# Kernel tuning notes

Hardware: AMD Instinct MI355X
Metric: run time of the kernel (lower is better)

Reference implementation:

```python
import jax, jax.numpy as jnp
import numpy as np

B, S, T_MEL, D, H = 16, 512, 2048, 256, 128  # batch, src_len, mel_len, encoder_hidden, lstm hidden/dir


def setup_inputs() -> dict:
    key = jax.random.key(0)
    ks = jax.random.split(key, 10)
    sc = 0.1
    x = jax.random.normal(ks[0], (B, S, D), jnp.float32)
    src_mask = jnp.zeros((B, S), bool)
    d = jax.random.uniform(ks[1], (B, S), jnp.float32, minval=0.5, maxval=8.0)
    duration = d / jnp.sum(d, -1, keepdims=True) * T_MEL  # each row sums exactly to mel_len
    Wih0 = sc * jax.random.normal(ks[2], (2, 4 * H, D), jnp.float32)
    Whh0 = sc * jax.random.normal(ks[3], (2, 4 * H, H), jnp.float32)
    b0 = jnp.zeros((2, 4 * H), jnp.float32)
    Wih1 = sc * jax.random.normal(ks[4], (2, 4 * H, 2 * H), jnp.float32)
    Whh1 = sc * jax.random.normal(ks[5], (2, 4 * H, H), jnp.float32)
    b1 = jnp.zeros((2, 4 * H), jnp.float32)
    proj_w = sc * jax.random.normal(ks[6], (1, 2 * H), jnp.float32)
    proj_b = jnp.zeros((1,), jnp.float32)
    return dict(x=x, src_mask=src_mask, duration=duration, Wih0=Wih0, Whh0=Whh0, b0=b0,
                Wih1=Wih1, Whh1=Whh1, b1=b1, proj_w=proj_w, proj_b=proj_b, mel_len=T_MEL)


def _lstm_dir(xt, Wih, Whh, b):
    # xt: [T, B, Din]; PyTorch gate order i, f, g, o
    Hh = Whh.shape[1]
    Bn = xt.shape[1]

    def step(carry, x_t):
        h, c = carry
        g = x_t @ Wih.T + h @ Whh.T + b
        i, f, gg, o = jnp.split(g, 4, axis=-1)
        c = jax.nn.sigmoid(f) * c + jax.nn.sigmoid(i) * jnp.tanh(gg)
        h = jax.nn.sigmoid(o) * jnp.tanh(c)
        return (h, c), h

    init = (jnp.zeros((Bn, Hh), xt.dtype), jnp.zeros((Bn, Hh), xt.dtype))
    _, hs = jax.lax.scan(step, init, xt)
    return hs  # [T, B, H]


def _bilstm_layer(x, Wih, Whh, b):
    # x: [B, S, Din] -> [B, S, 2H]
    xt = jnp.swapaxes(x, 0, 1)
    hf = _lstm_dir(xt, Wih[0], Whh[0], b[0])
    hb = _lstm_dir(xt[::-1], Wih[1], Whh[1], b[1])[::-1]
    return jnp.swapaxes(jnp.concatenate([hf, hb], -1), 0, 1)


def reference(x, src_mask, duration, Wih0, Whh0, b0, Wih1, Whh1, b1, proj_w, proj_b, mel_len):
    # ---- DurationPredictor: 2-layer BiLSTM + Linear + ReLU ----
    h = _bilstm_layer(x, Wih0, Whh0, b0)
    h = _bilstm_layer(h, Wih1, Whh1, b1)
    log_dur = jax.nn.relu(h @ proj_w.T + proj_b)[..., 0]  # [B, S]
    log_dur = jnp.where(src_mask, 0.0, log_dur)
    # ---- GaussianUpsampling with duration_target path ----
    e = jnp.cumsum(duration, -1)
    c = e - 0.5 * duration                                # [B, S]
    t = jnp.arange(1, mel_len + 1, dtype=jnp.float32)     # [T]
    w1 = jnp.exp(-0.1 * (t[None, None, :] - c[:, :, None]) ** 2)  # [B, S, T]
    w2 = jnp.sum(w1, axis=1, keepdims=True)
    w2 = jnp.where(w2 == 0.0, 1.0, w2)
    w = w1 / w2
    out = jnp.einsum('bst,bsd->btd', w, x)                # [B, T, D]
    return out, log_dur, duration, w
```

## Files before the change

### kernel.cpp

```cpp
#include <hip/hip_runtime.h>

#define B_ 16
#define S_ 512
#define T_ 2048
#define D_ 256
#define H_ 128

typedef _Float16 half2_t __attribute__((ext_vector_type(2)));
union U32H2 { unsigned u; half2_t h; };
union UH16 { _Float16 f; unsigned short u; };

#define WS_C     0
#define WS_W2    8192
#define WS_WPK   40960
#define WS_XG    303104
#define WS_H1    8691712

#define OUT_MAIN   0
#define OUT_LOGDUR 8388608
#define OUT_DUR    8396800
#define OUT_W      8404992

#define WAIT_LGKM0_ONLY 0xC07F

__device__ __forceinline__ unsigned packh2(float a, float b) {
    U32H2 u; u.h = half2_t{(_Float16)a, (_Float16)b}; return u.u;
}

template <int CTRL>
__device__ __forceinline__ float qswap(float v) {
    int i = __builtin_bit_cast(int, v);
    i = __builtin_amdgcn_update_dpp(0, i, CTRL, 0xf, 0xf, true);
    return __builtin_bit_cast(float, i);
}
#define QP_XOR1 0xB1
#define QP_XOR2 0x4E
#define QP_XOR3 0x1B

__global__ void prep_kernel(const float* __restrict__ dur, float* __restrict__ c,
                            float* __restrict__ out_dur) {
    int b = blockIdx.x;
    int s = threadIdx.x;
    __shared__ float sc[S_];
    float d = dur[b * S_ + s];
    sc[s] = d;
    __syncthreads();
    float v = d;
    for (int off = 1; off < S_; off <<= 1) {
        float add = (s >= off) ? sc[s - off] : 0.f;
        __syncthreads();
        v += add;
        sc[s] = v;
        __syncthreads();
    }
    c[b * S_ + s] = v - 0.5f * d;
    out_dur[b * S_ + s] = d;
}

__device__ void whh_pack_body(const float* __restrict__ Whh0, const float* __restrict__ Whh1,
                              unsigned* __restrict__ wpk, int gb) {
    int idx = gb * 256 + (int)threadIdx.x;
    int kk = idx & 15, g = (idx >> 4) & 3, st = (idx >> 6) & 511;
    int dir = (idx >> 15) & 1, layer = (idx >> 16) & 1;
    int e = st >> 2, q = st & 3;
    int row = g * 128 + e;
    int k2 = q * 16 + kk;
    const float* W = layer ? Whh1 : Whh0;
    wpk[idx] = packh2(W[dir * 65536 + row * 128 + 2 * k2],
                      W[dir * 65536 + row * 128 + 2 * k2 + 1]);
}

__device__ void wsum_body(const float* __restrict__ c, float* __restrict__ w2, int gb) {
    int idx = gb * 4 + ((int)threadIdx.x >> 6);
    int lane = threadIdx.x & 63;
    int b = idx >> 11, t = idx & 2047;
    float tv = (float)(t + 1);
    const float* cb = c + b * 512;
    float sum = 0.f;
#pragma unroll
    for (int i = 0; i < 8; i++) {
        float d = tv - cb[lane + 64 * i];
        sum += __expf(-0.1f * d * d);
    }
#pragma unroll
    for (int off = 32; off; off >>= 1) sum += __shfl_xor(sum, off);
    if (lane == 0) w2[idx] = (sum == 0.f) ? 1.f : sum;
}

#define BM 64
#define BN 64
#define BK 64
__device__ void gemm_xg_body(const float* __restrict__ A, const float* __restrict__ Bw,
                             const float* __restrict__ bias, float* __restrict__ Xg,
                             int bx, int by) {
    __shared__ float As[BK][BM + 4];
    __shared__ float Bs[BK][BN + 4];
    int tid = threadIdx.x;
    int m0 = bx * BM;
    int n0 = by * BN;
    int tm = tid >> 4, tn = tid & 15;
    float acc[4][4] = {};
    for (int k0 = 0; k0 < 256; k0 += BK) {
#pragma unroll
        for (int i = 0; i < 4; i++) {
            int p = tid + 256 * i;
            int m = p >> 4, kq = p & 15;
            float4 av = *reinterpret_cast<const float4*>(&A[(size_t)(m0 + m) * 256 + k0 + 4 * kq]);
            As[4 * kq + 0][m] = av.x; As[4 * kq + 1][m] = av.y;
            As[4 * kq + 2][m] = av.z; As[4 * kq + 3][m] = av.w;
            float4 bv = *reinterpret_cast<const float4*>(&Bw[(size_t)(n0 + m) * 256 + k0 + 4 * kq]);
            Bs[4 * kq + 0][m] = bv.x; Bs[4 * kq + 1][m] = bv.y;
            Bs[4 * kq + 2][m] = bv.z; Bs[4 * kq + 3][m] = bv.w;
        }
        __syncthreads();
#pragma unroll
        for (int k = 0; k < BK; k++) {
            float4 a4 = *reinterpret_cast<const float4*>(&As[k][4 * tm]);
            float4 b4 = *reinterpret_cast<const float4*>(&Bs[k][4 * tn]);
            float av[4] = {a4.x, a4.y, a4.z, a4.w};
            float bv[4] = {b4.x, b4.y, b4.z, b4.w};
#pragma unroll
            for (int i = 0; i < 4; i++)
#pragma unroll
                for (int j = 0; j < 4; j++) acc[i][j] += av[i] * bv[j];
        }
        __syncthreads();
    }
#pragma unroll
    for (int i = 0; i < 4; i++) {
        int m = m0 + 4 * tm + i;
        int b = m >> 9, s = m & 511;
#pragma unroll
        for (int jx = 0; jx < 4; jx++) {
            int n = n0 + 4 * tn + jx;
            int dir = n >> 9, jj = n & 511;
            Xg[((size_t)(dir * 512 + s) * 16 + b) * 512 + jj] = acc[i][jx] + bias[n];
        }
    }
}

__global__ __launch_bounds__(256) void stageA_kernel(const float* __restrict__ x,
                                                     const float* __restrict__ Wih0,
                                                     const float* __restrict__ b0,
                                                     float* __restrict__ Xg,
                                                     const float* __restrict__ Whh0,
                                                     const float* __restrict__ Whh1,
                                                     unsigned* __restrict__ wpk,
                                                     const float* __restrict__ c,
                                                     float* __restrict__ w2) {
    int blk = blockIdx.x;
    if (blk < 2048) {
        gemm_xg_body(x, Wih0, b0, Xg, blk & 127, blk >> 7);
    } else if (blk < 2560) {
        whh_pack_body(Whh0, Whh1, wpk, blk - 2048);
    } else {
        wsum_body(c, w2, blk - 2560);
    }
}

__global__ __launch_bounds__(256) void gemm_xg_kernel(const float* __restrict__ A,
                                                      const float* __restrict__ Bw,
                                                      const float* __restrict__ bias,
                                                      float* __restrict__ Xg) {
    gemm_xg_body(A, Bw, bias, Xg, blockIdx.x, blockIdx.y);
}

__device__ void lstm_scan_body(const float* __restrict__ Xg, const unsigned* __restrict__ wpk,
                               float* __restrict__ Hout, char* smem, int blk) {
    int dir = blk >> 4;
    int b = blk & 15;
    int st = threadIdx.x;
    int e = st >> 2, q = st & 3;

    const unsigned* wq = wpk + ((size_t)dir * 512 + st) * 64;
    uint4 w0, w1, w2, w3, w4, w5, w6, w7, w8, w9, w10, w11, w12, w13, w14, w15;
#define WL(W, OFF) \
    asm volatile("global_load_dwordx4 %0, %1, off offset:" #OFF : "=v"(W) : "v"(wq) : "memory")
    WL(w0, 0);    WL(w1, 16);   WL(w2, 32);   WL(w3, 48);
    WL(w4, 64);   WL(w5, 80);   WL(w6, 96);   WL(w7, 112);
    WL(w8, 128);  WL(w9, 144);  WL(w10, 160); WL(w11, 176);
    WL(w12, 192); WL(w13, 208); WL(w14, 224); WL(w15, 240);
#undef WL
    asm volatile("s_waitcnt vmcnt(0)" ::: "memory");

    unsigned short* hb = (unsigned short*)smem;
    if (st < 128) hb[st] = 0;

    float am = (q == 2) ? 2.f : 1.f;
    float ab = (q == 2) ? -1.f : 0.f;

    ptrdiff_t sstep = dir ? -8192 : 8192;
    int s0 = dir ? 511 : 0;
    const float* xg_p = Xg + (size_t)dir * (512 * 16 * 512) + (size_t)b * 512 + q * 128 + e
                        + (size_t)s0 * 8192;
    float xg_cur = xg_p[0];
    float xg_n1 = xg_p[sstep];
    const float* xg_pre = xg_p + 2 * sstep;
    float* ho_p = Hout + ((size_t)b * 512 + s0) * 256 + dir * 128 + e;
    ptrdiff_t hostep = dir ? -256 : 256;
    float c = 0.f;
    __syncthreads();

#define DOT4(ACC, WW, HH)                                                     \
        { U32H2 wa, wb, wc, wd, xa, xb, xc, xd;                               \
          wa.u = WW.x; wb.u = WW.y; wc.u = WW.z; wd.u = WW.w;                 \
          xa.u = HH.x; xb.u = HH.y; xc.u = HH.z; xd.u = HH.w;                 \
          ACC = __builtin_amdgcn_fdot2(xa.h, wa.h, ACC, false);               \
          ACC = __builtin_amdgcn_fdot2(xb.h, wb.h, ACC, false);               \
          ACC = __builtin_amdgcn_fdot2(xc.h, wc.h, ACC, false);               \
          ACC = __builtin_amdgcn_fdot2(xd.h, wd.h, ACC, false); }

#define SCAN_STEP(RDOFF, WROFF)                                               \
    {                                                                         \
        float xg_n2 = *xg_pre;                                                \
        xg_pre += sstep;                                                      \
        const uint4* h4 = (const uint4*)(hb + (RDOFF) + q * 32);              \
        uint4 h0 = h4[0], h1 = h4[1], h2 = h4[2], h3 = h4[3];                 \
        float a0 = 0.f, a1 = 0.f, a2 = 0.f, a3 = 0.f;                         \
        DOT4(a0, w0, h0)  DOT4(a0, w1, h1)  DOT4(a0, w2, h2)  DOT4(a0, w3, h3)\
        DOT4(a1, w4, h0)  DOT4(a1, w5, h1)  DOT4(a1, w6, h2)  DOT4(a1, w7, h3)\
        DOT4(a2, w8, h0)  DOT4(a2, w9, h1)  DOT4(a2, w10, h2) DOT4(a2, w11, h3)\
        DOT4(a3, w12, h0) DOT4(a3, w13, h1) DOT4(a3, w14, h2) DOT4(a3, w15, h3)\
        a0 += qswap<QP_XOR1>(a0); a0 += qswap<QP_XOR2>(a0);                   \
        a1 += qswap<QP_XOR1>(a1); a1 += qswap<QP_XOR2>(a1);                   \
        a2 += qswap<QP_XOR1>(a2); a2 += qswap<QP_XOR2>(a2);                   \
        a3 += qswap<QP_XOR1>(a3); a3 += qswap<QP_XOR2>(a3);                   \
        float gfull = (q == 0 ? a0 : q == 1 ? a1 : q == 2 ? a2 : a3) + xg_cur;\
        float sg = __builtin_amdgcn_rcpf(1.f + __expf(-(am * gfull)));        \
        float act = __builtin_fmaf(am, sg, ab);                               \
        float x1 = qswap<QP_XOR1>(act);                                       \
        float x2 = qswap<QP_XOR2>(act);                                       \
        float x3 = qswap<QP_XOR3>(act);                                       \
        if (q == 0) {                                                         \
            float cn = x1 * c + act * x2;                                     \
            c = cn;                                                           \
            float th = __builtin_fmaf(                                        \
                2.f, __builtin_amdgcn_rcpf(1.f + __expf(-2.f * cn)), -1.f);   \
            float h = x3 * th;                                                \
            UH16 hv; hv.f = (_Float16)h;                                      \
            hb[(WROFF) + e] = hv.u;                                           \
            *ho_p = h;                                                        \
        }                                                                     \
        ho_p += hostep;                                                       \
        __builtin_amdgcn_sched_barrier(0);                                    \
        __builtin_amdgcn_s_waitcnt(WAIT_LGKM0_ONLY);                          \
        __builtin_amdgcn_s_barrier();                                         \
        __builtin_amdgcn_sched_barrier(0);                                    \
        xg_cur = xg_n1;                                                       \
        xg_n1 = xg_n2;                                                        \
    }

    for (int it = 0; it < 256; it++) {
        SCAN_STEP(0, 128)
        SCAN_STEP(128, 0)
    }
#undef SCAN_STEP
#undef DOT4
}

__device__ void wwrite_body(const float* __restrict__ c, const float* __restrict__ w2,
                            float* __restrict__ wout, int gb) {
    int base = (gb * 512 + (int)threadIdx.x) * 8;
    int t0 = base & 2047;
    int bs = base >> 11;
    int b = bs >> 9;
    float cv = c[bs];
    float4 w2a = *(const float4*)&w2[b * 2048 + t0];
    float4 w2b = *(const float4*)&w2[b * 2048 + t0 + 4];
    float r[8];
#pragma unroll
    for (int i = 0; i < 8; i++) {
        float d = (float)(t0 + 1 + i) - cv;
        r[i] = __expf(-0.1f * d * d);
    }
    float4 o1 = {r[0] / w2a.x, r[1] / w2a.y, r[2] / w2a.z, r[3] / w2a.w};
    float4 o2 = {r[4] / w2b.x, r[5] / w2b.y, r[6] / w2b.z, r[7] / w2b.w};
    *(float4*)&wout[base] = o1;
    *(float4*)&wout[base + 4] = o2;
}

__device__ void gemm_out_body(const float* __restrict__ wmat, const float* __restrict__ x,
                              float* __restrict__ out, int gb, char* smem) {
    int tt = gb & 15, dd = (gb >> 4) & 3, b = gb >> 6;
    int m0 = tt * 128, n0 = dd * 64;
    unsigned* As2 = (unsigned*)smem;
    unsigned* Bs2 = As2 + 32 * 136;
    const float* wb = wmat + (size_t)b * (512 * 2048);
    const float* xb = x + (size_t)b * (512 * 256);
    int tid = threadIdx.x;
    int tm = tid >> 4, tn = tid & 15;
    float acc[4][4] = {};
    for (int k0 = 0; k0 < 512; k0 += 64) {
#pragma unroll
        for (int i = 0; i < 2; i++) {
            int p = tid + 512 * i;
            int k2 = p >> 5, mq = p & 31;
            float4 lo = *(const float4*)&wb[(size_t)(k0 + 2 * k2) * 2048 + m0 + 4 * mq];
            float4 hi = *(const float4*)&wb[(size_t)(k0 + 2 * k2 + 1) * 2048 + m0 + 4 * mq];
            uint4 o;
            o.x = packh2(lo.x, hi.x); o.y = packh2(lo.y, hi.y);
            o.z = packh2(lo.z, hi.z); o.w = packh2(lo.w, hi.w);
            *(uint4*)&As2[k2 * 136 + 4 * mq] = o;
        }
        {
            int k2 = tid >> 4, nq = tid & 15;
            float4 lo = *(const float4*)&xb[(size_t)(k0 + 2 * k2) * 256 + n0 + 4 * nq];
            float4 hi = *(const float4*)&xb[(size_t)(k0 + 2 * k2 + 1) * 256 + n0 + 4 * nq];
            uint4 o;
            o.x = packh2(lo.x, hi.x); o.y = packh2(lo.y, hi.y);
            o.z = packh2(lo.z, hi.z); o.w = packh2(lo.w, hi.w);
            *(uint4*)&Bs2[k2 * 72 + 4 * nq] = o;
        }
        __syncthreads();
#pragma unroll
        for (int k2 = 0; k2 < 32; k2++) {
            uint4 a4 = *(const uint4*)&As2[k2 * 136 + 4 * tm];
            uint4 b4 = *(const uint4*)&Bs2[k2 * 72 + 4 * tn];
            U32H2 aa0, aa1, aa2, aa3, bb0, bb1, bb2, bb3;
            aa0.u = a4.x; aa1.u = a4.y; aa2.u = a4.z; aa3.u = a4.w;
            bb0.u = b4.x; bb1.u = b4.y; bb2.u = b4.z; bb3.u = b4.w;
            half2_t av[4] = {aa0.h, aa1.h, aa2.h, aa3.h};
            half2_t bv[4] = {bb0.h, bb1.h, bb2.h, bb3.h};
#pragma unroll
            for (int i = 0; i < 4; i++)
#pragma unroll
                for (int j = 0; j < 4; j++)
                    acc[i][j] = __builtin_amdgcn_fdot2(av[i], bv[j], acc[i][j], false);
        }
        __syncthreads();
    }
#pragma unroll
    for (int i = 0; i < 4; i++) {
        int m = m0 + 4 * tm + i;
        float4 o = {acc[i][0], acc[i][1], acc[i][2], acc[i][3]};
        *(float4*)&out[((size_t)b * 2048 + m) * 256 + n0 + 4 * tn] = o;
    }
}

__global__ __launch_bounds__(512) __attribute__((amdgpu_waves_per_eu(2, 2)))
void fusedA_kernel(const float* __restrict__ Xg, const unsigned* __restrict__ wpk,
                   float* __restrict__ H1, const float* __restrict__ c,
                   const float* __restrict__ w2, float* __restrict__ out_w) {
    extern __shared__ char smem[];
    if (blockIdx.x < 32) lstm_scan_body(Xg, wpk, H1, smem, blockIdx.x);
    else wwrite_body(c, w2, out_w, blockIdx.x - 32);
}

__global__ __launch_bounds__(512) __attribute__((amdgpu_waves_per_eu(2, 2)))
void fusedB_kernel(const float* __restrict__ Xg, const unsigned* __restrict__ wpk,
                   float* __restrict__ H1, const float* __restrict__ wmat,
                   const float* __restrict__ x, float* __restrict__ out_main) {
    extern __shared__ char smem[];
    if (blockIdx.x < 32) lstm_scan_body(Xg, wpk, H1, smem, blockIdx.x);
    else gemm_out_body(wmat, x, out_main, blockIdx.x - 32, smem);
}

__global__ void proj_kernel(const float* __restrict__ H2, const float* __restrict__ pw,
                            const float* __restrict__ pb, const unsigned char* __restrict__ mask,
                            float* __restrict__ out) {
    int row = blockIdx.x * 4 + (threadIdx.x >> 6);
    int lane = threadIdx.x & 63;
    float4 h = *reinterpret_cast<const float4*>(&H2[(size_t)row * 256 + lane * 4]);
    float4 w = *reinterpret_cast<const float4*>(&pw[lane * 4]);
    float v = h.x * w.x + h.y * w.y + h.z * w.z + h.w * w.w;
#pragma unroll
    for (int off = 32; off; off >>= 1) v += __shfl_xor(v, off);
    if (lane == 0) {
        float r = v + pb[0];
        r = r > 0.f ? r : 0.f;
        if (mask[row]) r = 0.f;
        out[row] = r;
    }
}

extern "C" void kernel_launch(void* const* d_in, const int* in_sizes, int n_in,
                              void* d_out, int out_size, void* d_ws, size_t ws_size,
                              hipStream_t stream) {
    const float* x = (const float*)d_in[0];
    const unsigned char* mask = (const unsigned char*)d_in[1];
    const float* dur = (const float*)d_in[2];
    const float* Wih0 = (const float*)d_in[3];
    const float* Whh0 = (const float*)d_in[4];
    const float* b0 = (const float*)d_in[5];
    const float* Wih1 = (const float*)d_in[6];
    const float* Whh1 = (const float*)d_in[7];
    const float* b1 = (const float*)d_in[8];
    const float* pw = (const float*)d_in[9];
    const float* pb = (const float*)d_in[10];

    float* out = (float*)d_out;
    float* ws = (float*)d_ws;
    float* c = ws + WS_C;
    float* w2 = ws + WS_W2;
    unsigned* wpk = (unsigned*)(ws + WS_WPK);
    float* Xg = ws + WS_XG;
    float* H1 = ws + WS_H1;

    float* out_main = out + OUT_MAIN;
    float* out_logdur = out + OUT_LOGDUR;
    float* out_dur = out + OUT_DUR;
    float* out_w = out + OUT_W;

    prep_kernel<<<16, 512, 0, stream>>>(dur, c, out_dur);

    stageA_kernel<<<2048 + 512 + 8192, 256, 0, stream>>>(x, Wih0, b0, Xg,
                                                         Whh0, Whh1, wpk, c, w2);

    fusedA_kernel<<<32 + 4096, 512, 1024, stream>>>(Xg, wpk, H1, c, w2, out_w);

    gemm_xg_kernel<<<dim3(128, 16), 256, 0, stream>>>(H1, Wih1, b1, Xg);
    fusedB_kernel<<<32 + 1024, 512, 26624, stream>>>(Xg, wpk + 65536, H1, out_w, x, out_main);

    proj_kernel<<<2048, 256, 0, stream>>>(H1, pw, pb, mask, out_logdur);
}
```

Before: 656.8 us.

## Split LSTM recurrent dot products across 8 lanes with 1024-thread blocks

After: 852.9 us. +29.9%, slower.

```diff
diff --git a/kernel.cpp b/kernel.cpp
--- a/kernel.cpp
+++ b/kernel.cpp
@@ -60,11 +60,11 @@
 __device__ void whh_pack_body(const float* __restrict__ Whh0, const float* __restrict__ Whh1,
                               unsigned* __restrict__ wpk, int gb) {
     int idx = gb * 256 + (int)threadIdx.x;
-    int kk = idx & 15, g = (idx >> 4) & 3, st = (idx >> 6) & 511;
+    int kk = idx & 7, g = (idx >> 3) & 3, st = (idx >> 5) & 1023;
     int dir = (idx >> 15) & 1, layer = (idx >> 16) & 1;
-    int e = st >> 2, q = st & 3;
+    int e = st >> 3, r = st & 7;
     int row = g * 128 + e;
-    int k2 = q * 16 + kk;
+    int k2 = r * 8 + kk;
     const float* W = layer ? Whh1 : Whh0;
     wpk[idx] = packh2(W[dir * 65536 + row * 128 + 2 * k2],
                       W[dir * 65536 + row * 128 + 2 * k2 + 1]);
@@ -170,28 +170,27 @@
     int dir = blk >> 4;
     int b = blk & 15;
     int st = threadIdx.x;
-    int e = st >> 2, q = st & 3;
-
-    const unsigned* wq = wpk + ((size_t)dir * 512 + st) * 64;
-    uint4 w0, w1, w2, w3, w4, w5, w6, w7, w8, w9, w10, w11, w12, w13, w14, w15;
+    int e = st >> 3, r = st & 7;
+    int sel = r & 3;
+
+    const unsigned* wq = wpk + ((size_t)dir * 1024 + st) * 32;
+    uint4 w0, w1, w2, w3, w4, w5, w6, w7;
 #define WL(W, OFF) \
     asm volatile("global_load_dwordx4 %0, %1, off offset:" #OFF : "=v"(W) : "v"(wq) : "memory")
-    WL(w0, 0);    WL(w1, 16);   WL(w2, 32);   WL(w3, 48);
-    WL(w4, 64);   WL(w5, 80);   WL(w6, 96);   WL(w7, 112);
-    WL(w8, 128);  WL(w9, 144);  WL(w10, 160); WL(w11, 176);
-    WL(w12, 192); WL(w13, 208); WL(w14, 224); WL(w15, 240);
+    WL(w0, 0);  WL(w1, 16); WL(w2, 32); WL(w3, 48);
+    WL(w4, 64); WL(w5, 80); WL(w6, 96); WL(w7, 112);
 #undef WL
     asm volatile("s_waitcnt vmcnt(0)" ::: "memory");
 
     unsigned short* hb = (unsigned short*)smem;
     if (st < 128) hb[st] = 0;
 
-    float am = (q == 2) ? 2.f : 1.f;
-    float ab = (q == 2) ? -1.f : 0.f;
+    float am = (sel == 2) ? 2.f : 1.f;
+    float ab = (sel == 2) ? -1.f : 0.f;
 
     ptrdiff_t sstep = dir ? -8192 : 8192;
     int s0 = dir ? 511 : 0;
-    const float* xg_p = Xg + (size_t)dir * (512 * 16 * 512) + (size_t)b * 512 + q * 128 + e
+    const float* xg_p = Xg + (size_t)dir * (512 * 16 * 512) + (size_t)b * 512 + sel * 128 + e
                         + (size_t)s0 * 8192;
     float xg_cur = xg_p[0];
     float xg_n1 = xg_p[sstep];
@@ -214,24 +213,26 @@
     {                                                                         \
         float xg_n2 = *xg_pre;                                                \
         xg_pre += sstep;                                                      \
-        const uint4* h4 = (const uint4*)(hb + (RDOFF) + q * 32);              \
-        uint4 h0 = h4[0], h1 = h4[1], h2 = h4[2], h3 = h4[3];                 \
+        const uint4* h4 = (const uint4*)(hb + (RDOFF) + r * 16);              \
+        uint4 ha = h4[0], hc = h4[1];                                         \
         float a0 = 0.f, a1 = 0.f, a2 = 0.f, a3 = 0.f;                         \
-        DOT4(a0, w0, h0)  DOT4(a0, w1, h1)  DOT4(a0, w2, h2)  DOT4(a0, w3, h3)\
-        DOT4(a1, w4, h0)  DOT4(a1, w5, h1)  DOT4(a1, w6, h2)  DOT4(a1, w7, h3)\
-        DOT4(a2, w8, h0)  DOT4(a2, w9, h1)  DOT4(a2, w10, h2) DOT4(a2, w11, h3)\
-        DOT4(a3, w12, h0) DOT4(a3, w13, h1) DOT4(a3, w14, h2) DOT4(a3, w15, h3)\
+        DOT4(a0, w0, ha) DOT4(a0, w1, hc)                                     \
+        DOT4(a1, w2, ha) DOT4(a1, w3, hc)                                     \
+        DOT4(a2, w4, ha) DOT4(a2, w5, hc)                                     \
+        DOT4(a3, w6, ha) DOT4(a3, w7, hc)                                     \
         a0 += qswap<QP_XOR1>(a0); a0 += qswap<QP_XOR2>(a0);                   \
         a1 += qswap<QP_XOR1>(a1); a1 += qswap<QP_XOR2>(a1);                   \
         a2 += qswap<QP_XOR1>(a2); a2 += qswap<QP_XOR2>(a2);                   \
         a3 += qswap<QP_XOR1>(a3); a3 += qswap<QP_XOR2>(a3);                   \
-        float gfull = (q == 0 ? a0 : q == 1 ? a1 : q == 2 ? a2 : a3) + xg_cur;\
+        float p = (sel == 0 ? a0 : sel == 1 ? a1 : sel == 2 ? a2 : a3);       \
+        p += __shfl_xor(p, 4);                                                \
+        float gfull = p + xg_cur;                                             \
         float sg = __builtin_amdgcn_rcpf(1.f + __expf(-(am * gfull)));        \
         float act = __builtin_fmaf(am, sg, ab);                               \
         float x1 = qswap<QP_XOR1>(act);                                       \
         float x2 = qswap<QP_XOR2>(act);                                       \
         float x3 = qswap<QP_XOR3>(act);                                       \
-        if (q == 0) {                                                         \
+        if (r == 0) {                                                         \
             float cn = x1 * c + act * x2;                                     \
             c = cn;                                                           \
             float th = __builtin_fmaf(                                        \
@@ -260,7 +261,7 @@
 
 __device__ void wwrite_body(const float* __restrict__ c, const float* __restrict__ w2,
                             float* __restrict__ wout, int gb) {
-    int base = (gb * 512 + (int)threadIdx.x) * 8;
+    int base = (gb * 1024 + (int)threadIdx.x) * 8;
     int t0 = base & 2047;
     int bs = base >> 11;
     int b = bs >> 9;
@@ -281,20 +282,18 @@
 
 __device__ void gemm_out_body(const float* __restrict__ wmat, const float* __restrict__ x,
                               float* __restrict__ out, int gb, char* smem) {
-    int tt = gb & 15, dd = (gb >> 4) & 3, b = gb >> 6;
-    int m0 = tt * 128, n0 = dd * 64;
+    int tt = gb & 15, dd = (gb >> 4) & 1, b = gb >> 5;
+    int m0 = tt * 128, n0 = dd * 128;
     unsigned* As2 = (unsigned*)smem;
     unsigned* Bs2 = As2 + 32 * 136;
     const float* wb = wmat + (size_t)b * (512 * 2048);
     const float* xb = x + (size_t)b * (512 * 256);
     int tid = threadIdx.x;
-    int tm = tid >> 4, tn = tid & 15;
+    int tm = tid >> 5, tn = tid & 31;
     float acc[4][4] = {};
     for (int k0 = 0; k0 < 512; k0 += 64) {
-#pragma unroll
-        for (int i = 0; i < 2; i++) {
-            int p = tid + 512 * i;
-            int k2 = p >> 5, mq = p & 31;
+        {
+            int k2 = tid >> 5, mq = tid & 31;
             float4 lo = *(const float4*)&wb[(size_t)(k0 + 2 * k2) * 2048 + m0 + 4 * mq];
             float4 hi = *(const float4*)&wb[(size_t)(k0 + 2 * k2 + 1) * 2048 + m0 + 4 * mq];
             uint4 o;
@@ -303,19 +302,19 @@
             *(uint4*)&As2[k2 * 136 + 4 * mq] = o;
         }
         {
-            int k2 = tid >> 4, nq = tid & 15;
+            int k2 = tid >> 5, nq = tid & 31;
             float4 lo = *(const float4*)&xb[(size_t)(k0 + 2 * k2) * 256 + n0 + 4 * nq];
             float4 hi = *(const float4*)&xb[(size_t)(k0 + 2 * k2 + 1) * 256 + n0 + 4 * nq];
             uint4 o;
             o.x = packh2(lo.x, hi.x); o.y = packh2(lo.y, hi.y);
             o.z = packh2(lo.z, hi.z); o.w = packh2(lo.w, hi.w);
-            *(uint4*)&Bs2[k2 * 72 + 4 * nq] = o;
+            *(uint4*)&Bs2[k2 * 136 + 4 * nq] = o;
         }
         __syncthreads();
 #pragma unroll
         for (int k2 = 0; k2 < 32; k2++) {
             uint4 a4 = *(const uint4*)&As2[k2 * 136 + 4 * tm];
-            uint4 b4 = *(const uint4*)&Bs2[k2 * 72 + 4 * tn];
+            uint4 b4 = *(const uint4*)&Bs2[k2 * 136 + 4 * tn];
             U32H2 aa0, aa1, aa2, aa3, bb0, bb1, bb2, bb3;
             aa0.u = a4.x; aa1.u = a4.y; aa2.u = a4.z; aa3.u = a4.w;
             bb0.u = b4.x; bb1.u = b4.y; bb2.u = b4.z; bb3.u = b4.w;
@@ -337,7 +336,7 @@
     }
 }
 
-__global__ __launch_bounds__(512) __attribute__((amdgpu_waves_per_eu(2, 2)))
+__global__ __launch_bounds__(1024) __attribute__((amdgpu_waves_per_eu(4, 4)))
 void fusedA_kernel(const float* __restrict__ Xg, const unsigned* __restrict__ wpk,
                    float* __restrict__ H1, const float* __restrict__ c,
                    const float* __restrict__ w2, float* __restrict__ out_w) {
@@ -346,7 +345,7 @@
     else wwrite_body(c, w2, out_w, blockIdx.x - 32);
 }
 
-__global__ __launch_bounds__(512) __attribute__((amdgpu_waves_per_eu(2, 2)))
+__global__ __launch_bounds__(1024) __attribute__((amdgpu_waves_per_eu(4, 4)))
 void fusedB_kernel(const float* __restrict__ Xg, const unsigned* __restrict__ wpk,
                    float* __restrict__ H1, const float* __restrict__ wmat,
                    const float* __restrict__ x, float* __restrict__ out_main) {
@@ -406,10 +405,10 @@
     stageA_kernel<<<2048 + 512 + 8192, 256, 0, stream>>>(x, Wih0, b0, Xg,
                                                          Whh0, Whh1, wpk, c, w2);
 
-    fusedA_kernel<<<32 + 4096, 512, 1024, stream>>>(Xg, wpk, H1, c, w2, out_w);
+    fusedA_kernel<<<32 + 2048, 1024, 1024, stream>>>(Xg, wpk, H1, c, w2, out_w);
 
     gemm_xg_kernel<<<dim3(128, 16), 256, 0, stream>>>(H1, Wih1, b1, Xg);
-    fusedB_kernel<<<32 + 1024, 512, 26624, stream>>>(Xg, wpk + 65536, H1, out_w, x, out_main);
+    fusedB_kernel<<<32 + 512, 1024, 34816, stream>>>(Xg, wpk + 65536, H1, out_w, x, out_main);
 
     proj_kernel<<<2048, 256, 0, stream>>>(H1, pw, pb, mask, out_logdur);
 }
```
